# Kernel tuning notes

Hardware: AMD Instinct MI355X
Metric: run time of the kernel (lower is better)

## Reference

```python
import jax, jax.numpy as jnp
import numpy as np

LN_EPS = 1e-5


def layer_norm(x, g, b):
    mu = jnp.mean(x, axis=-1, keepdims=True)
    var = jnp.var(x, axis=-1, keepdims=True)
    return (x - mu) / jnp.sqrt(var + LN_EPS) * g + b


def balanced_assignment(scores):
    # scores: [T, E]. Assign exactly C = T//E tokens to each expert,
    # greedily per expert by affinity (emulates libbase.balanced_assignment's
    # equal-split output structure deterministically).
    T, E = scores.shape
    C = T // E
    taken = jnp.zeros((T,), dtype=bool)
    parts = []
    for e in range(E):  # small fixed loop over experts
        s = jnp.where(taken, -jnp.inf, scores[:, e])
        _, idx = jax.lax.top_k(s, C)
        parts.append(idx)
        taken = taken.at[idx].set(True)
    return jnp.concatenate(parts)  # [T], chunks of C tokens per expert


def setup_inputs() -> dict:
    key = jax.random.key(0)
    ks = jax.random.split(key, 4)
    B, S, D, F, E = 4, 2048, 1024, 4096, 8
    return {
        "x": jax.random.normal(ks[0], (B, S, D), dtype=jnp.float32),
        "centroids": jax.random.normal(ks[1], (E, D), dtype=jnp.float32) * 0.1,
        "ln_g": jnp.ones((D,), dtype=jnp.float32),
        "ln_b": jnp.zeros((D,), dtype=jnp.float32),
        "w1": jax.random.normal(ks[2], (E, D, F), dtype=jnp.float32) * 0.02,
        "b1": jnp.zeros((E, F), dtype=jnp.float32),
        "w2": jax.random.normal(ks[3], (E, F, D), dtype=jnp.float32) * 0.02,
        "b2": jnp.zeros((E, D), dtype=jnp.float32),
    }


def reference(x, centroids, ln_g, ln_b, w1, b1, w2, b2):
    D = x.shape[-1]
    feat = x.reshape(-1, D)                      # [T, D]
    T = feat.shape[0]
    E = centroids.shape[0]
    C = T // E

    # affinity scores under no_grad in the original
    norm = layer_norm(feat, ln_g, ln_b)
    scores = jax.lax.stop_gradient(norm @ centroids.T)   # [T, E]

    sort_by_expert = balanced_assignment(scores)          # [T]

    routed = feat[sort_by_expert].reshape(E, C, D)        # dispatch gather

    # expert FFN sublayer: residual + W2(gelu(W1(ln(x))))
    h = layer_norm(routed, ln_g, ln_b)
    h = jax.nn.gelu(jnp.einsum('ecd,edf->ecf', h, w1) + b1[:, None, :])
    h = jnp.einsum('ecf,efd->ecd', h, w2) + b2[:, None, :]
    out = routed + h                                      # [E, C, D]

    # inverse_sort scatter: undo the dispatch permutation
    inv = jnp.zeros((T,), dtype=jnp.int32).at[sort_by_expert].set(
        jnp.arange(T, dtype=jnp.int32))
    return out.reshape(T, D)[inv].reshape(x.shape)
```

## Files before the change

### kernel.cpp

```cpp
#include <hip/hip_runtime.h>
#include <hip/hip_bf16.h>
#include <stdint.h>


#define T_TOK 8192
#define DM    1024
#define FF    4096
#define NE    8
#define CAP   1024

typedef __attribute__((ext_vector_type(8))) __bf16 bf16x8;
typedef __attribute__((ext_vector_type(4))) float  f32x4;

__device__ __forceinline__ unsigned short f2bf(float f) {
  unsigned u = __float_as_uint(f);
  u += 0x7FFFu + ((u >> 16) & 1u);
  return (unsigned short)(u >> 16);
}
__device__ __forceinline__ unsigned keyu(float s) {
  unsigned bb = __float_as_uint(s);
  return (bb & 0x80000000u) ? ~bb : (bb | 0x80000000u);
}
__device__ __forceinline__ void gload_lds16(const void* g, void* l) {
  __builtin_amdgcn_global_load_lds(
      (const __attribute__((address_space(1))) unsigned int*)(uintptr_t)g,
      (__attribute__((address_space(3))) unsigned int*)l, 16, 0, 0);
}

__global__ __launch_bounds__(256) void ln_scores_k(
    const float* __restrict__ x, const float* __restrict__ g,
    const float* __restrict__ b, const float* __restrict__ cent,
    unsigned short* __restrict__ nrm, float* __restrict__ scores) {
  const int t = blockIdx.x, tid = threadIdx.x;
  const int lane = tid & 63, w = tid >> 6;
  float4 v = ((const float4*)(x + (size_t)t * DM))[tid];
  float f0 = v.x, f1 = v.y, f2 = v.z, f3 = v.w;
  float s = f0 + f1 + f2 + f3;
  float sq = f0 * f0 + f1 * f1 + f2 * f2 + f3 * f3;
#pragma unroll
  for (int o = 32; o > 0; o >>= 1) { s += __shfl_xor(s, o); sq += __shfl_xor(sq, o); }
  __shared__ float red[8];
  if (lane == 0) { red[w] = s; red[4 + w] = sq; }
  __syncthreads();
  float S = red[0] + red[1] + red[2] + red[3];
  float SQ = red[4] + red[5] + red[6] + red[7];
  float mu = S * (1.0f / DM);
  float var = SQ * (1.0f / DM) - mu * mu;
  float rstd = rsqrtf(var + 1e-5f);
  float4 gv = ((const float4*)g)[tid];
  float4 bv = ((const float4*)b)[tid];
  float n0 = (f0 - mu) * rstd * gv.x + bv.x;
  float n1 = (f1 - mu) * rstd * gv.y + bv.y;
  float n2 = (f2 - mu) * rstd * gv.z + bv.z;
  float n3 = (f3 - mu) * rstd * gv.w + bv.w;
  ushort4 o4;
  o4.x = f2bf(n0); o4.y = f2bf(n1); o4.z = f2bf(n2); o4.w = f2bf(n3);
  ((ushort4*)(nrm + (size_t)t * DM))[tid] = o4;
  __shared__ float sred[4];
  for (int e = 0; e < NE; ++e) {
    float4 cv = ((const float4*)(cent + e * DM))[tid];
    float p = n0 * cv.x + n1 * cv.y + n2 * cv.z + n3 * cv.w;
#pragma unroll
    for (int o = 32; o > 0; o >>= 1) p += __shfl_xor(p, o);
    if (lane == 0) sred[w] = p;
    __syncthreads();
    if (tid == 0) scores[(size_t)e * T_TOK + t] = sred[0] + sred[1] + sred[2] + sred[3];
    __syncthreads();
  }
}

__device__ __forceinline__ void pivot_scan(const unsigned* hist, unsigned* S,
                                           int l) {
  unsigned v0 = hist[4 * l], v1 = hist[4 * l + 1];
  unsigned v2 = hist[4 * l + 2], v3 = hist[4 * l + 3];
  unsigned own = v0 + v1 + v2 + v3;
  unsigned s = own;
#pragma unroll
  for (int off = 1; off < 64; off <<= 1) {
    unsigned t = __shfl_down(s, off);
    if (l + off < 64) s += t;
  }
  unsigned i3 = (s - own) + v3;
  unsigned i2 = i3 + v2;
  unsigned i1 = i2 + v1;
  unsigned i0 = i1 + v0;
  unsigned need = S[0];
  if (i0 >= need && i0 - v0 < need) { S[1] = 4 * l + 0; S[0] = need - (i0 - v0); }
  if (i1 >= need && i1 - v1 < need) { S[1] = 4 * l + 1; S[0] = need - (i1 - v1); }
  if (i2 >= need && i2 - v2 < need) { S[1] = 4 * l + 2; S[0] = need - (i2 - v2); }
  if (i3 >= need && i3 - v3 < need) { S[1] = 4 * l + 3; S[0] = need - (i3 - v3); }
}
__device__ __forceinline__ void tie_select(const unsigned* bmap, unsigned* S,
                                           int* tokdst, unsigned char* taken,
                                           int l) {
  unsigned wds[4] = {bmap[4 * l], bmap[4 * l + 1], bmap[4 * l + 2], bmap[4 * l + 3]};
  unsigned cnt = __popc(wds[0]) + __popc(wds[1]) + __popc(wds[2]) + __popc(wds[3]);
  unsigned p = cnt;
#pragma unroll
  for (int off = 1; off < 64; off <<= 1) {
    unsigned t = __shfl_up(p, off);
    if (l >= off) p += t;
  }
  unsigned base = p - cnt;
  const unsigned r = S[0];
#pragma unroll
  for (int c = 0; c < 4; ++c) {
    unsigned word = wds[c];
    while (word && base < r) {
      int b = __ffs(word) - 1; word &= word - 1;
      int i = (4 * l + c) * 32 + b;
      unsigned pp = atomicAdd(&S[2], 1u);
      tokdst[pp] = i; taken[i] = 1;
      ++base;
    }
    base += __popc(word);
  }
}

__device__ void assign_body(const float* __restrict__ scores,
                            int* __restrict__ tok, char* smem) {
  unsigned*       key   = (unsigned*)smem;
  unsigned short* candA = (unsigned short*)(smem + 32768);
  unsigned short* candB = (unsigned short*)(smem + 49152);
  unsigned char*  taken = (unsigned char*)(smem + 65536);
  unsigned*       h0    = (unsigned*)(smem + 73728);
  unsigned*       h1    = (unsigned*)(smem + 74752);
  unsigned*       h2    = (unsigned*)(smem + 75776);
  unsigned*       h3    = (unsigned*)(smem + 76800);
  unsigned*       bmap  = (unsigned*)(smem + 77824);
  unsigned*       S     = (unsigned*)(smem + 78848);
  const int tid = threadIdx.x;
  for (int i = tid; i < T_TOK; i += 1024) taken[i] = 0;
  if (tid < 256) h0[tid] = 0;
  __syncthreads();
  for (int e = 0; e < NE; ++e) {
    const float* se = scores + (size_t)e * T_TOK;
    if (tid == 0) { S[0] = CAP; S[2] = 0; S[4] = 0; }
    else if (tid >= 256 && tid < 512) h1[tid - 256] = 0;
    __syncthreads();
    unsigned kreg[8];
    {
      float sc[8];
      unsigned char tk[8];
#pragma unroll
      for (int j = 0; j < 8; ++j) sc[j] = se[j * 1024 + tid];
#pragma unroll
      for (int j = 0; j < 8; ++j) tk[j] = taken[j * 1024 + tid];
#pragma unroll
      for (int j = 0; j < 8; ++j) {
        unsigned k = tk[j] ? 0u : keyu(sc[j]);
        kreg[j] = k;
        key[j * 1024 + tid] = k;
        atomicAdd(&h0[k >> 24], 1u);
      }
    }
    __syncthreads();
    if (tid < 64) pivot_scan(h0, S, tid);
    else if (tid >= 256 && tid < 512) h2[tid - 256] = 0;
    __syncthreads();
    if (tid < 256) h0[tid] = 0;
    {
      const unsigned pb = S[1];
#pragma unroll
      for (int j = 0; j < 8; ++j) {
        int i = j * 1024 + tid;
        unsigned k = kreg[j];
        unsigned by = k >> 24;
        if (by > pb) {
          unsigned p = atomicAdd(&S[2], 1u);
          tok[e * CAP + p] = i; taken[i] = 1;
        } else if (by == pb) {
          unsigned q = atomicAdd(&S[4], 1u);
          candA[q] = (unsigned short)i;
          atomicAdd(&h1[(k >> 16) & 255u], 1u);
        }
      }
    }
    __syncthreads();
    if (tid < 64) pivot_scan(h1, S, tid);
    else if (tid == 64) S[5] = 0;
    else if (tid >= 256 && tid < 512) h3[tid - 256] = 0;
    __syncthreads();
    {
      const unsigned m = S[4], pb = S[1];
      for (unsigned q = tid; q < m; q += 1024) {
        unsigned i = candA[q];
        unsigned k = key[i];
        unsigned by = (k >> 16) & 255u;
        if (by > pb) {
          unsigned p = atomicAdd(&S[2], 1u);
          tok[e * CAP + p] = (int)i; taken[i] = 1;
        } else if (by == pb) {
          unsigned p = atomicAdd(&S[5], 1u);
          candB[p] = (unsigned short)i;
          atomicAdd(&h2[(k >> 8) & 255u], 1u);
        }
      }
    }
    __syncthreads();
    if (tid < 64) pivot_scan(h2, S, tid);
    else if (tid == 64) S[4] = 0;
    __syncthreads();
    {
      const unsigned m = S[5], pb = S[1];
      for (unsigned q = tid; q < m; q += 1024) {
        unsigned i = candB[q];
        unsigned k = key[i];
        unsigned by = (k >> 8) & 255u;
        if (by > pb) {
          unsigned p = atomicAdd(&S[2], 1u);
          tok[e * CAP + p] = (int)i; taken[i] = 1;
        } else if (by == pb) {
          unsigned p = atomicAdd(&S[4], 1u);
          candA[p] = (unsigned short)i;
          atomicAdd(&h3[k & 255u], 1u);
        }
      }
    }
    __syncthreads();
    if (tid < 64) pivot_scan(h3, S, tid);
    else if (tid >= 256 && tid < 512) bmap[tid - 256] = 0;
    __syncthreads();
    {
      const unsigned m = S[4], pb = S[1];
      for (unsigned q = tid; q < m; q += 1024) {
        unsigned i = candA[q];
        unsigned by = key[i] & 255u;
        if (by > pb) {
          unsigned p = atomicAdd(&S[2], 1u);
          tok[e * CAP + p] = (int)i; taken[i] = 1;
        } else if (by == pb) {
          atomicOr(&bmap[i >> 5], 1u << (i & 31));
        }
      }
    }
    __syncthreads();
    if (tid < 64) tie_select(bmap, S, tok + e * CAP, taken, tid);
    __syncthreads();
  }
}

__global__ __launch_bounds__(1024) void fat_assign_transpose(
    const float* __restrict__ scores, int* __restrict__ tok,
    const float* __restrict__ w1, const float* __restrict__ w2,
    unsigned short* __restrict__ w1T, unsigned short* __restrict__ w2T) {
  __shared__ __align__(16) char smem[79872];
  if (blockIdx.x == 0) { assign_body(scores, tok, smem); return; }
  const int tix = blockIdx.x - 1;
  const int which = tix >> 11;
  const int r = tix & 2047;
  const int e = r >> 8;
  const int rr = r & 255;
  int K, N, nt, kt;
  const float* s;
  unsigned short* d;
  if (which == 0) { K = DM; N = FF; nt = rr & 31; kt = rr >> 5; s = w1; d = w1T; }
  else            { K = FF; N = DM; nt = rr & 7;  kt = rr >> 3; s = w2; d = w2T; }
  s += (size_t)e * K * N;
  d += (size_t)e * N * K;
  const int q = threadIdx.x >> 8, t2 = threadIdx.x & 255;
  const int k0 = kt * 128 + (q >> 1) * 64;
  const int n0 = nt * 128 + (q & 1) * 64;
  float (*t)[65] = (float (*)[65])(smem + q * 16640);
  for (int p = t2; p < 1024; p += 256) {
    int rw = p >> 4, c4 = (p & 15) * 4;
    float4 v = *(const float4*)(s + (size_t)(k0 + rw) * N + n0 + c4);
    t[c4 + 0][rw] = v.x; t[c4 + 1][rw] = v.y;
    t[c4 + 2][rw] = v.z; t[c4 + 3][rw] = v.w;
  }
  __syncthreads();
  for (int p = t2; p < 512; p += 256) {
    int c = p >> 3, r8 = (p & 7) * 8;
    unsigned short tmp[8];
#pragma unroll
    for (int i = 0; i < 8; ++i) tmp[i] = f2bf(t[c][r8 + i]);
    *(uint4*)(d + (size_t)(n0 + c) * K + k0 + r8) = *(const uint4*)tmp;
  }
}

template <int EPI, bool GATHER, int K, int N, int BM, int BN, int TPB,
          int WM, int WN>
__global__ __launch_bounds__(TPB, 2) void gemm_ring(
    const unsigned short* __restrict__ A, const unsigned short* __restrict__ Bt,
    const float* __restrict__ bias, const int* __restrict__ tok,
    const float* __restrict__ xres, void* __restrict__ Cout) {
  constexpr int NT  = K / 32;
  constexpr int RM  = BM / WM, RN = BN / WN;
  constexpr int MR  = RM / 16, NR = RN / 16;
  constexpr int ALD = (BM * 32) / (8 * TPB);
  constexpr int BLD = (BN * 32) / (8 * TPB);
  constexpr int LD  = ALD + BLD;
  constexpr int SLOT = (BM + BN) * 32;
  __shared__ __align__(16) unsigned short lds[3 * SLOT];
  __shared__ int tokl[BM];

  const int flat = blockIdx.x + gridDim.x * (blockIdx.y + gridDim.y * blockIdx.z);
  const int nwg = gridDim.x * gridDim.y * gridDim.z;
  const int nf = (flat & 7) * (nwg >> 3) + (flat >> 3);
  const int bx = nf % gridDim.x;
  const int rem = nf / gridDim.x;
  const int e  = rem / gridDim.y;
  const int n0 = bx * BN, m0 = (rem % gridDim.y) * BM;

  const int tid = threadIdx.x, lane = tid & 63, w = tid >> 6;
  const int wr = w / WN, wc = w % WN;
  const int lr = lane & 15, lk = lane >> 4;

  for (int i = tid; i < BM; i += TPB) tokl[i] = tok[e * CAP + m0 + i];
  __syncthreads();

  const unsigned short* aptr[ALD];
  const unsigned short* bptr[BLD];
  const unsigned short* Be = Bt + (size_t)e * N * K + (size_t)n0 * K;
#pragma unroll
  for (int i = 0; i < ALD; ++i) {
    int c = i * TPB + tid, row = c >> 2, sp = c & 3;
    int s = sp ^ ((row >> 1) & 3);
    size_t grow = GATHER ? (size_t)tokl[row] : (size_t)(e * CAP + m0 + row);
    aptr[i] = A + grow * K + s * 8;
  }
#pragma unroll
  for (int i = 0; i < BLD; ++i) {
    int c = i * TPB + tid, row = c >> 2, sp = c & 3;
    int s = sp ^ ((row >> 1) & 3);
    bptr[i] = Be + (size_t)row * K + s * 8;
  }
  auto stage = [&](int tile, int slot) {
    unsigned short* base = lds + (size_t)slot * SLOT;
#pragma unroll
    for (int i = 0; i < ALD; ++i)
      gload_lds16(aptr[i] + tile * 32, base + (i * TPB + tid) * 8);
#pragma unroll
    for (int i = 0; i < BLD; ++i)
      gload_lds16(bptr[i] + tile * 32, base + BM * 32 + (i * TPB + tid) * 8);
  };

  const int swz = (lr >> 1) & 3;
  const int afo = (wr * RM + lr) * 32 + (lk ^ swz) * 8;
  const int bfo = BM * 32 + (wc * RN + lr) * 32 + (lk ^ swz) * 8;

  f32x4 acc[MR][NR] = {};

  stage(0, 0); stage(1, 1);
  asm volatile("s_waitcnt vmcnt(%0)" :: "i"(LD) : "memory");
  __builtin_amdgcn_s_barrier();

  int slot = 0;
#pragma unroll 1
  for (int t = 0; t < NT; ++t) {
    const unsigned short* base = lds + (size_t)slot * SLOT;
    bf16x8 af[MR], bfr[NR];
#pragma unroll
    for (int mi = 0; mi < MR; ++mi)
      af[mi] = *(const bf16x8*)(base + afo + mi * 512);
#pragma unroll
    for (int ni = 0; ni < NR; ++ni)
      bfr[ni] = *(const bf16x8*)(base + bfo + ni * 512);
    if (t + 2 < NT) {
      int dst = slot - 1;
      if (dst < 0) dst = 2;
      stage(t + 2, dst);
      asm volatile("s_waitcnt vmcnt(%0)" :: "i"(LD) : "memory");
    } else if (t + 2 == NT) {
      asm volatile("s_waitcnt vmcnt(0)" ::: "memory");
    }
    __builtin_amdgcn_s_barrier();
    asm volatile("s_waitcnt lgkmcnt(0)" ::: "memory");
    __builtin_amdgcn_sched_barrier(0);
    __builtin_amdgcn_s_setprio(1);
#pragma unroll
    for (int mi = 0; mi < MR; ++mi)
#pragma unroll
      for (int ni = 0; ni < NR; ++ni)
        acc[mi][ni] = __builtin_amdgcn_mfma_f32_16x16x32_bf16(
            af[mi], bfr[ni], acc[mi][ni], 0, 0, 0);
    __builtin_amdgcn_s_setprio(0);
    __builtin_amdgcn_s_barrier();
    slot = (slot == 2) ? 0 : slot + 1;
  }

  const int lg = lane >> 4;
#pragma unroll
  for (int ni = 0; ni < NR; ++ni) {
    const int n = n0 + wc * RN + ni * 16 + lr;
    const float bb = bias[e * N + n];
#pragma unroll
    for (int mi = 0; mi < MR; ++mi) {
#pragma unroll
      for (int r = 0; r < 4; ++r) {
        const int ml = wr * RM + mi * 16 + lg * 4 + r;
        float v = acc[mi][ni][r] + bb;
        if (EPI == 1) {
          float z = 1.5957691216f * v + 0.07135481283f * v * v * v;
          float gl = v / (1.0f + __expf(-z));
          ((unsigned short*)Cout)[(size_t)(e * CAP + m0 + ml) * N + n] = f2bf(gl);
        } else {
          const int token = tokl[ml];
          v += xres[(size_t)token * DM + n];
          ((float*)Cout)[(size_t)token * (size_t)N + n] = v;
        }
      }
    }
  }
}

extern "C" void kernel_launch(void* const* d_in, const int* in_sizes, int n_in,
                              void* d_out, int out_size, void* d_ws, size_t ws_size,
                              hipStream_t stream) {
  const float* x    = (const float*)d_in[0];
  const float* cent = (const float*)d_in[1];
  const float* ln_g = (const float*)d_in[2];
  const float* ln_b = (const float*)d_in[3];
  const float* w1   = (const float*)d_in[4];
  const float* b1   = (const float*)d_in[5];
  const float* w2   = (const float*)d_in[6];
  const float* b2   = (const float*)d_in[7];
  float* out = (float*)d_out;

  char* ws = (char*)d_ws;
  size_t off = 0;
  unsigned short* w1T = (unsigned short*)(ws + off); off += (size_t)NE * FF * DM * 2;
  unsigned short* w2T = (unsigned short*)(ws + off); off += (size_t)NE * DM * FF * 2;
  unsigned short* nrm = (unsigned short*)(ws + off); off += (size_t)T_TOK * DM * 2;
  unsigned short* h1  = (unsigned short*)(ws + off); off += (size_t)T_TOK * FF * 2;
  float* scores       = (float*)(ws + off);          off += (size_t)NE * T_TOK * 4;
  int* tok            = (int*)(ws + off);            off += (size_t)T_TOK * 4;

  ln_scores_k<<<dim3(T_TOK), 256, 0, stream>>>(x, ln_g, ln_b, cent, nrm, scores);
  fat_assign_transpose<<<dim3(1 + 4096), 1024, 0, stream>>>(
      scores, tok, w1, w2, w1T, w2T);
  gemm_ring<1, true, DM, FF, 256, 128, 512, 4, 2>
      <<<dim3(FF / 128, CAP / 256, NE), 512, 0, stream>>>(nrm, w1T, b1, tok, nullptr, h1);
  gemm_ring<2, false, FF, DM, 128, 128, 256, 2, 2>
      <<<dim3(DM / 128, CAP / 128, NE), 256, 0, stream>>>(h1, w2T, b2, tok, x, out);
}
```

Before: 300.6 us.

## Fuse layernorm-score pass into assign/transpose kernel with atomic counter handoff

Removes the separate layernorm+scores launch and folds it into the fat kernel as 2048 extra blocks, each handling four tokens with 1024 threads. Block 0, which runs the balanced assignment, spin-waits on a global counter until all layernorm blocks have finished. The weight-transpose blocks can then overlap with the layernorm and assignment work. This trades one launch boundary for a spin-wait, and it relies on block 0 not starving the layernorm blocks of scheduling slots, which risks a deadlock if they cannot become resident.

```diff
diff --git a/kernel.cpp b/kernel.cpp
--- a/kernel.cpp
+++ b/kernel.cpp
@@ -27,44 +27,48 @@
       (__attribute__((address_space(3))) unsigned int*)l, 16, 0, 0);
 }
 
-__global__ __launch_bounds__(256) void ln_scores_k(
-    const float* __restrict__ x, const float* __restrict__ g,
-    const float* __restrict__ b, const float* __restrict__ cent,
-    unsigned short* __restrict__ nrm, float* __restrict__ scores) {
-  const int t = blockIdx.x, tid = threadIdx.x;
-  const int lane = tid & 63, w = tid >> 6;
-  float4 v = ((const float4*)(x + (size_t)t * DM))[tid];
+__device__ void ln_group(const float* __restrict__ x, const float* __restrict__ g,
+                         const float* __restrict__ b, const float* __restrict__ cent,
+                         unsigned short* __restrict__ nrm, float* __restrict__ scores,
+                         int t, char* smem) {
+  float (*red)[8]  = (float (*)[8])smem;
+  float (*sred)[4] = (float (*)[4])(smem + 128);
+  const int tid = threadIdx.x;
+  const int grp = tid >> 8, tg = tid & 255;
+  const int lane = tid & 63, w = (tid >> 6) & 3;
+  float4 v = ((const float4*)(x + (size_t)t * DM))[tg];
   float f0 = v.x, f1 = v.y, f2 = v.z, f3 = v.w;
   float s = f0 + f1 + f2 + f3;
   float sq = f0 * f0 + f1 * f1 + f2 * f2 + f3 * f3;
 #pragma unroll
   for (int o = 32; o > 0; o >>= 1) { s += __shfl_xor(s, o); sq += __shfl_xor(sq, o); }
-  __shared__ float red[8];
-  if (lane == 0) { red[w] = s; red[4 + w] = sq; }
+  __shared__ float dummy_guard;
+  if (lane == 0) { red[grp][w] = s; red[grp][4 + w] = sq; }
   __syncthreads();
-  float S = red[0] + red[1] + red[2] + red[3];
-  float SQ = red[4] + red[5] + red[6] + red[7];
+  float S = red[grp][0] + red[grp][1] + red[grp][2] + red[grp][3];
+  float SQ = red[grp][4] + red[grp][5] + red[grp][6] + red[grp][7];
   float mu = S * (1.0f / DM);
   float var = SQ * (1.0f / DM) - mu * mu;
   float rstd = rsqrtf(var + 1e-5f);
-  float4 gv = ((const float4*)g)[tid];
-  float4 bv = ((const float4*)b)[tid];
+  float4 gv = ((const float4*)g)[tg];
+  float4 bv = ((const float4*)b)[tg];
   float n0 = (f0 - mu) * rstd * gv.x + bv.x;
   float n1 = (f1 - mu) * rstd * gv.y + bv.y;
   float n2 = (f2 - mu) * rstd * gv.z + bv.z;
   float n3 = (f3 - mu) * rstd * gv.w + bv.w;
   ushort4 o4;
   o4.x = f2bf(n0); o4.y = f2bf(n1); o4.z = f2bf(n2); o4.w = f2bf(n3);
-  ((ushort4*)(nrm + (size_t)t * DM))[tid] = o4;
-  __shared__ float sred[4];
+  ((ushort4*)(nrm + (size_t)t * DM))[tg] = o4;
   for (int e = 0; e < NE; ++e) {
-    float4 cv = ((const float4*)(cent + e * DM))[tid];
+    float4 cv = ((const float4*)(cent + e * DM))[tg];
     float p = n0 * cv.x + n1 * cv.y + n2 * cv.z + n3 * cv.w;
 #pragma unroll
     for (int o = 32; o > 0; o >>= 1) p += __shfl_xor(p, o);
-    if (lane == 0) sred[w] = p;
-    __syncthreads();
-    if (tid == 0) scores[(size_t)e * T_TOK + t] = sred[0] + sred[1] + sred[2] + sred[3];
+    if (lane == 0) sred[grp][w] = p;
+    __syncthreads();
+    if (tg == 0)
+      scores[(size_t)e * T_TOK + t] =
+          sred[grp][0] + sred[grp][1] + sred[grp][2] + sred[grp][3];
     __syncthreads();
   }
 }
@@ -240,13 +244,34 @@
   }
 }
 
-__global__ __launch_bounds__(1024) void fat_assign_transpose(
-    const float* __restrict__ scores, int* __restrict__ tok,
+#define LN_BLOCKS 2048
+__global__ __launch_bounds__(1024) void fat_all(
+    const float* __restrict__ x, const float* __restrict__ ln_g,
+    const float* __restrict__ ln_b, const float* __restrict__ cent,
+    unsigned short* __restrict__ nrm, float* __restrict__ scores,
+    int* __restrict__ tok, unsigned* __restrict__ ctr,
     const float* __restrict__ w1, const float* __restrict__ w2,
     unsigned short* __restrict__ w1T, unsigned short* __restrict__ w2T) {
   __shared__ __align__(16) char smem[79872];
-  if (blockIdx.x == 0) { assign_body(scores, tok, smem); return; }
-  const int tix = blockIdx.x - 1;
+  const int bid = blockIdx.x;
+  if (bid == 0) {
+    if (threadIdx.x == 0) {
+      while (atomicAdd(ctr, 0u) < LN_BLOCKS) __builtin_amdgcn_s_sleep(8);
+      __threadfence();
+    }
+    __syncthreads();
+    assign_body(scores, tok, smem);
+    return;
+  }
+  if (bid <= LN_BLOCKS) {
+    const int t = (bid - 1) * 4 + (threadIdx.x >> 8);
+    ln_group(x, ln_g, ln_b, cent, nrm, scores, t, smem);
+    if ((threadIdx.x & 255) == 0) __threadfence();
+    __syncthreads();
+    if (threadIdx.x == 0) atomicAdd(ctr, 1u);
+    return;
+  }
+  const int tix = bid - 1 - LN_BLOCKS;
   const int which = tix >> 11;
   const int r = tix & 2047;
   const int e = r >> 8;
@@ -425,10 +450,11 @@
   unsigned short* h1  = (unsigned short*)(ws + off); off += (size_t)T_TOK * FF * 2;
   float* scores       = (float*)(ws + off);          off += (size_t)NE * T_TOK * 4;
   int* tok            = (int*)(ws + off);            off += (size_t)T_TOK * 4;
-
-  ln_scores_k<<<dim3(T_TOK), 256, 0, stream>>>(x, ln_g, ln_b, cent, nrm, scores);
-  fat_assign_transpose<<<dim3(1 + 4096), 1024, 0, stream>>>(
-      scores, tok, w1, w2, w1T, w2T);
+  unsigned* ctr       = (unsigned*)(ws + off);       off += 64;
+
+  hipMemsetAsync(ctr, 0, 4, stream);
+  fat_all<<<dim3(1 + LN_BLOCKS + 4096), 1024, 0, stream>>>(
+      x, ln_g, ln_b, cent, nrm, scores, tok, ctr, w1, w2, w1T, w2T);
   gemm_ring<1, true, DM, FF, 256, 128, 512, 4, 2>
       <<<dim3(FF / 128, CAP / 256, NE), 512, 0, stream>>>(nrm, w1T, b1, tok, nullptr, h1);
   gemm_ring<2, false, FF, DM, 128, 128, 256, 2, 2>
```

Result: slower. 467.1 us (+55.4%).
